# Performance work log

Measured on AMD Instinct MI355X. Metric: run time of the kernel, lower is better.

Reference implementation:

```python
import jax, jax.numpy as jnp
from jax import lax
import numpy as np
import math

ALPHA = 1000.0
BETA = 100.0
K = 24
INIT_DIM = 64
STAGES = 4
NUM_POINTS = 2048
B = 16
EPS = 1e-5


def embedding_spe(x, out_dim):
    # x: [..., in_dim] -> [..., out_dim] sinusoidal embedding
    in_dim = x.shape[-1]
    feat_dim = math.ceil(out_dim / (in_dim * 2))
    dim_embed = jnp.asarray(ALPHA ** (np.arange(feat_dim) / feat_dim), x.dtype)
    feat_num = feat_dim * 2 * in_dim
    out_idx = np.linspace(0, feat_num - 1, out_dim).astype(np.int64)
    div = BETA * x[..., None] / dim_embed            # [..., in_dim, feat_dim]
    pe = jnp.stack([jnp.sin(div), jnp.cos(div)], -1)  # [..., in_dim, feat_dim, 2]
    pe = pe.reshape(x.shape[:-1] + (feat_num,))       # order matches torch cat(flatten(stack))
    return pe[..., out_idx]


def fps_single(xyz, npoint):
    # xyz: [N,3] -> indices [npoint] (deterministic start at index 0)
    n = xyz.shape[0]

    def body(carry, _):
        dist, farthest = carry
        centroid = xyz[farthest]
        d = jnp.sum((xyz - centroid) ** 2, -1)
        dist = jnp.minimum(dist, d)
        nxt = jnp.argmax(dist).astype(jnp.int32)
        return (dist, nxt), farthest

    init = (jnp.full((n,), 1e10, xyz.dtype), jnp.array(0, jnp.int32))
    _, idx = lax.scan(body, init, None, length=npoint)
    return idx


def knn(k, xyz, new_xyz):
    # xyz [B,N,3], new_xyz [B,S,3] -> [B,S,k] indices of k nearest points
    d = (jnp.sum(new_xyz ** 2, -1, keepdims=True)
         + jnp.sum(xyz ** 2, -1)[:, None, :]
         - 2.0 * jnp.einsum('bsc,bnc->bsn', new_xyz, xyz))
    _, idx = lax.top_k(-d, k)
    return idx


def gather(pts, idx):
    # pts [B,N,C], idx [B,...] -> [B,...,C]
    b = pts.shape[0]
    bi = jnp.arange(b).reshape((b,) + (1,) * (idx.ndim - 1))
    return pts[bi, idx]


def stage(xyz, feat, npoint, out_dim, gamma, beta_p):
    fps_idx = jax.vmap(lambda p: fps_single(p, npoint))(lax.stop_gradient(xyz))
    xyz_s = gather(xyz, fps_idx)    # [B,S,3]
    feat_s = gather(feat, fps_idx)  # [B,S,C]
    idx_knn = knn(K, lax.stop_gradient(xyz), lax.stop_gradient(xyz_s))  # [B,S,K]
    xyz_knn = gather(xyz, idx_knn)    # [B,S,K,3]
    feat_knn = gather(feat, idx_knn)  # [B,S,K,C]
    # normalize by global (unbiased) std, like torch.std over whole tensor
    xyz_c = xyz_knn - xyz_s[:, :, None, :]
    xyz_knn = xyz_c / (jnp.std(xyz_c, ddof=1) + 1e-05)
    feat_c = feat_knn - feat_s[:, :, None, :]
    feat_knn = feat_c / (jnp.std(feat_c, ddof=1) + 1e-05)
    bsz, s, k, c = feat_knn.shape
    feat_knn = jnp.concatenate(
        [feat_knn, jnp.broadcast_to(feat_s[:, :, None, :], (bsz, s, k, c))], -1)  # [B,S,K,2C]
    # SPE aggregation
    pe = embedding_spe(xyz_knn, out_dim)
    w = (feat_knn + pe) * pe
    # neighbor pooling: max + mean over K
    agg = jnp.max(w, -2) + jnp.mean(w, -2)  # [B,S,out_dim]
    # BatchNorm1d (training-mode batch stats, biased var) + exact GELU
    mean = jnp.mean(agg, axis=(0, 1))
    var = jnp.var(agg, axis=(0, 1))
    y = gamma * (agg - mean) / jnp.sqrt(var + EPS) + beta_p
    return xyz_s, jax.nn.gelu(y, approximate=False)


def setup_inputs() -> dict:
    key = jax.random.key(0)
    ks = jax.random.split(key, 2)
    inp = {'xyz': jax.random.normal(ks[0], (B, NUM_POINTS, 3), jnp.float32)}
    dim = INIT_DIM
    for i in range(STAGES):
        dim *= 2
        inp[f'gamma{i}'] = jnp.ones((dim,), jnp.float32)
        inp[f'beta{i}'] = jnp.zeros((dim,), jnp.float32)
    return inp


def reference(xyz, gamma0, beta0, gamma1, beta1, gamma2, beta2, gamma3, beta3):
    gammas = [gamma0, gamma1, gamma2, gamma3]
    betas = [beta0, beta1, beta2, beta3]
    feat = embedding_spe(xyz, INIT_DIM)
    npoint, dim = NUM_POINTS, INIT_DIM
    for i in range(STAGES):
        dim *= 2
        npoint //= 2
        xyz, feat = stage(xyz, feat, npoint, dim, gammas[i], betas[i])
    return jnp.max(feat, -2) + jnp.mean(feat, -2)  # [B, 1024]
```

## Files before the change

### kernel.cpp

```cpp
#include <hip/hip_runtime.h>
#include <math.h>

#pragma clang fp contract(off)

static constexpr int BATCH = 16;
static constexpr int NPTS0 = 2048;
static constexpr int KNN = 24;

static constexpr size_t OFF_STATS = 0;
static constexpr size_t OFF_BN    = 256;
static constexpr size_t OFF_DE    = 32768;
static constexpr size_t OFF_MAP   = 36864;
static constexpr size_t OFF_XYZ1  = 49152;
static constexpr size_t OFF_XYZ2  = OFF_XYZ1 + (size_t)16*1024*3*4;
static constexpr size_t OFF_XYZ3  = OFF_XYZ2 + (size_t)16*512*3*4;
static constexpr size_t OFF_XYZ4  = OFF_XYZ3 + (size_t)16*256*3*4;
static constexpr size_t OFF_FPS0  = OFF_XYZ4 + (size_t)16*128*3*4;
static constexpr size_t OFF_FPS1  = OFF_FPS0 + (size_t)16*1024*4;
static constexpr size_t OFF_FPS2  = OFF_FPS1 + (size_t)16*512*4;
static constexpr size_t OFF_FPS3  = OFF_FPS2 + (size_t)16*256*4;
static constexpr size_t OFF_KNN   = OFF_FPS3 + (size_t)16*128*4;
static constexpr size_t OFF_FEATA = OFF_KNN + (size_t)16*1024*24*4;
static constexpr size_t OFF_FEATB = OFF_FEATA + (size_t)16*2048*64*4;
static constexpr size_t OFF_FEATS = OFF_FEATB + (size_t)16*2048*64*4;
static constexpr size_t OFF_AGG   = OFF_FEATS + (size_t)16*1024*64*4;
static constexpr size_t WS_NEED   = OFF_AGG + (size_t)16*1024*128*4;

__device__ inline uint64_t kmax64(uint64_t a, uint64_t b) { return a > b ? a : b; }

template <int CTRL>
__device__ inline uint64_t dpp_shift64(uint64_t k) {
  int hi = (int)(unsigned)(k >> 32), lo = (int)(unsigned)k;
  int oh = __builtin_amdgcn_update_dpp(hi, hi, CTRL, 0xF, 0xF, false);
  int ol = __builtin_amdgcn_update_dpp(lo, lo, CTRL, 0xF, 0xF, false);
  return ((uint64_t)(unsigned)oh << 32) | (unsigned)ol;
}
__device__ inline uint64_t wave_reduce_max64(uint64_t k) {
  k = kmax64(k, dpp_shift64<0x111>(k));
  k = kmax64(k, dpp_shift64<0x112>(k));
  k = kmax64(k, dpp_shift64<0x114>(k));
  k = kmax64(k, dpp_shift64<0x118>(k));
  k = kmax64(k, dpp_shift64<0x142>(k));
  k = kmax64(k, dpp_shift64<0x143>(k));
  return k;
}

__device__ inline unsigned sortable_f32(float f) {
  unsigned b = __float_as_uint(f);
  unsigned m = (unsigned)((int)b >> 31) | 0x80000000u;
  return b ^ m;
}

__device__ inline unsigned med3u(unsigned a, unsigned b, unsigned c) {
  unsigned r;
  asm("v_med3_u32 %0, %1, %2, %3" : "=v"(r) : "v"(a), "v"(b), "v"(c));
  return r;
}

__device__ inline void ins24(unsigned kk[KNN], unsigned v) {
#pragma unroll
  for (int e = KNN - 1; e >= 1; --e) kk[e] = med3u(kk[e - 1], kk[e], v);
  kk[0] = kk[0] < v ? kk[0] : v;
}

__global__ void init_tables(float* __restrict__ de, int* __restrict__ mp) {
  const int outs[5] = {64, 128, 256, 512, 1024};
  const int fds[5]  = {11, 22, 43, 86, 171};
  const int deo[5]  = {0, 11, 33, 76, 162};
  const int mpo[5]  = {0, 64, 192, 448, 960};
  const int tid = threadIdx.x;
  for (int c = 0; c < 5; ++c) {
    const int fd = fds[c], out = outs[c];
    for (int j = tid; j < fd; j += blockDim.x)
      de[deo[c] + j] = (float)pow(1000.0, (double)j / (double)fd);
    const double step = (double)(6 * fd - 1) / (double)(out - 1);
    for (int f = tid; f < out; f += blockDim.x)
      mp[mpo[c] + f] = (int)(step * (double)f);
  }
}

__global__ __launch_bounds__(256) void embed_init(const float* __restrict__ xyz,
                                                  float* __restrict__ feat,
                                                  const float* __restrict__ de,
                                                  const int* __restrict__ mp) {
  int g = blockIdx.x * blockDim.x + threadIdx.x;
  if (g >= BATCH * NPTS0 * 64) return;
  int c = g & 63;
  int bn = g >> 6;
  int m = mp[c];
  int sc = m & 1;
  int a = m >> 1;
  int ci = a / 11;
  int j = a - ci * 11;
  float x = xyz[bn * 3 + ci];
  float ang = (100.0f * x) / de[j];
  feat[g] = sc ? cosf(ang) : sinf(ang);
}

template <int PTS>
__device__ void fps_stage(const float* lds_cur, float* lds_next, int* idx_buf,
                          unsigned* red,
                          int* __restrict__ fps_idx, float* __restrict__ xyz_next) {
  const int S = PTS * 128;
  const int tid = threadIdx.x;
  float px[PTS], py[PTS], pz[PTS], dist[PTS];
#pragma unroll
  for (int p = 0; p < PTS; ++p) {
    int gi = tid + p * 256;
    px[p] = lds_cur[3 * gi];
    py[p] = lds_cur[3 * gi + 1];
    pz[p] = lds_cur[3 * gi + 2];
    dist[p] = 1e10f;
  }
  float cx = lds_cur[0], cy = lds_cur[1], cz = lds_cur[2];
  if (tid == 0) {
    idx_buf[0] = 0;
    lds_next[0] = cx; lds_next[1] = cy; lds_next[2] = cz;
  }
  for (int t = 1; t < S; ++t) {
    float bd = -1.0f;
    int bp = 0;
#pragma unroll
    for (int p = 0; p < PTS; ++p) {
      float dx = px[p] - cx, dy = py[p] - cy, dz = pz[p] - cz;
      float dd = dx * dx + dy * dy;
      dd = dd + dz * dz;
      float nd = fminf(dist[p], dd);
      dist[p] = nd;
      if (nd > bd) { bd = nd; bp = p; }
    }
    unsigned gi = (unsigned)tid + ((unsigned)bp << 8);
    uint64_t key = ((uint64_t)__float_as_uint(bd) << 32) | (~gi);
    key = wave_reduce_max64(key);
    unsigned wlo = (unsigned)__builtin_amdgcn_readlane((int)(unsigned)key, 63);
    unsigned whi = (unsigned)__builtin_amdgcn_readlane((int)(unsigned)(key >> 32), 63);
    unsigned gi_w = ~wlo;
    unsigned pw = gi_w >> 8;
    float wx = px[0], wy = py[0], wz = pz[0];
#pragma unroll
    for (int p = 1; p < PTS; ++p)
      if (pw == (unsigned)p) { wx = px[p]; wy = py[p]; wz = pz[p]; }
    if (tid == (int)(gi_w & 255u)) {
      unsigned* row = red + (t & 1) * 32 + (tid >> 6) * 8;
      row[0] = whi; row[1] = wlo;
      row[2] = __float_as_uint(wx); row[3] = __float_as_uint(wy); row[4] = __float_as_uint(wz);
    }
    __syncthreads();
    const unsigned* rp = red + (t & 1) * 32;
    uint4 q0 = *(const uint4*)(rp + 0);
    uint4 q1 = *(const uint4*)(rp + 8);
    uint4 q2 = *(const uint4*)(rp + 16);
    uint4 q3 = *(const uint4*)(rp + 24);
    unsigned z0 = rp[4], z1 = rp[12], z2 = rp[20], z3 = rp[28];
    uint64_t k0 = ((uint64_t)q0.x << 32) | q0.y;
    uint64_t k1 = ((uint64_t)q1.x << 32) | q1.y;
    uint64_t k2 = ((uint64_t)q2.x << 32) | q2.y;
    uint64_t k3 = ((uint64_t)q3.x << 32) | q3.y;
    bool s01 = k0 >= k1;
    uint64_t ka = s01 ? k0 : k1;
    unsigned xa = s01 ? q0.z : q1.z, ya = s01 ? q0.w : q1.w, za = s01 ? z0 : z1;
    bool s23 = k2 >= k3;
    uint64_t kb = s23 ? k2 : k3;
    unsigned xb = s23 ? q2.z : q3.z, yb = s23 ? q2.w : q3.w, zb = s23 ? z2 : z3;
    bool sab = ka >= kb;
    uint64_t km = sab ? ka : kb;
    cx = __uint_as_float(sab ? xa : xb);
    cy = __uint_as_float(sab ? ya : yb);
    cz = __uint_as_float(sab ? za : zb);
    if (tid == 0) {
      idx_buf[t] = (int)(~(unsigned)km);
      lds_next[3 * t] = cx; lds_next[3 * t + 1] = cy; lds_next[3 * t + 2] = cz;
    }
  }
  __syncthreads();
  for (int u = tid; u < S; u += 256) fps_idx[u] = idx_buf[u];
  for (int u = tid; u < 3 * S; u += 256) xyz_next[u] = lds_next[u];
}

__global__ __launch_bounds__(256) void fps_all(const float* __restrict__ xyz0,
                                               float* __restrict__ xyz1, float* __restrict__ xyz2,
                                               float* __restrict__ xyz3, float* __restrict__ xyz4,
                                               int* __restrict__ i0, int* __restrict__ i1,
                                               int* __restrict__ i2, int* __restrict__ i3) {
  __shared__ float lds[3 * (2048 + 1024 + 512 + 256 + 128)];
  __shared__ int idxb[1024 + 512 + 256 + 128];
  __shared__ __align__(16) unsigned red[2 * 4 * 8];
  const int b = blockIdx.x;
  float* l0 = lds;
  float* l1 = l0 + 3 * 2048;
  float* l2 = l1 + 3 * 1024;
  float* l3 = l2 + 3 * 512;
  float* l4 = l3 + 3 * 256;
  int* ib0 = idxb;
  int* ib1 = ib0 + 1024;
  int* ib2 = ib1 + 512;
  int* ib3 = ib2 + 256;
  for (int t = threadIdx.x; t < 3 * 2048; t += 256) l0[t] = xyz0[(size_t)b * 3 * 2048 + t];
  __syncthreads();
  fps_stage<8>(l0, l1, ib0, red, i0 + b * 1024, xyz1 + (size_t)b * 1024 * 3);
  fps_stage<4>(l1, l2, ib1, red, i1 + b * 512, xyz2 + (size_t)b * 512 * 3);
  fps_stage<2>(l2, l3, ib2, red, i2 + b * 256, xyz3 + (size_t)b * 256 * 3);
  fps_stage<1>(l3, l4, ib3, red, i3 + b * 128, xyz4 + (size_t)b * 128 * 3);
}

static constexpr int MGS = 29;
__global__ __launch_bounds__(256) void knn_tau(const float* __restrict__ db_xyz,
                                               const float* __restrict__ q_xyz,
                                               unsigned* __restrict__ tau,
                                               int Np, int S) {
  extern __shared__ float smem[];
  float4* db = (float4*)smem;
  unsigned* mg = (unsigned*)(db + Np);
  const int tid = threadIdx.x, lane = tid & 63, wv = tid >> 6;
  const int bpb = S >> 6;
  const int b = blockIdx.x / bpb;
  const int qbase = (blockIdx.x % bpb) * 64;
  for (int j = tid; j < Np; j += 256) {
    float x = db_xyz[((size_t)b * Np + j) * 3 + 0];
    float y = db_xyz[((size_t)b * Np + j) * 3 + 1];
    float z = db_xyz[((size_t)b * Np + j) * 3 + 2];
    float pn = x * x + y * y;
    pn = pn + z * z;
    db[j] = make_float4(x, y, z, pn);
  }
  __syncthreads();
  const int s = qbase + lane;
  float qx = q_xyz[((size_t)b * S + s) * 3 + 0];
  float qy = q_xyz[((size_t)b * S + s) * 3 + 1];
  float qz = q_xyz[((size_t)b * S + s) * 3 + 2];
  float qn = qx * qx + qy * qy;
  qn = qn + qz * qz;
  unsigned kk[KNN];
#pragma unroll
  for (int e = 0; e < KNN; ++e) kk[e] = 0xFFFFFFFFu;
  const int cpw = Np >> 2;
  const int beg = wv * cpw, end = beg + cpw;
  for (int j0 = beg; j0 < end; j0 += 8) {
    float4 p[8];
#pragma unroll
    for (int u = 0; u < 8; ++u) p[u] = db[j0 + u];
#pragma unroll
    for (int u = 0; u < 8; ++u) {
      float dot = fmaf(qz, p[u].z, fmaf(qy, p[u].y, qx * p[u].x));
      float d = (qn + p[u].w) - 2.0f * dot;
      unsigned su = sortable_f32(d);
      if (__any(su < kk[KNN - 1])) ins24(kk, su);
    }
  }
  unsigned* myrow = mg + (wv * 64 + lane) * MGS;
#pragma unroll
  for (int e = 0; e < KNN; ++e) myrow[e] = kk[e];
  __syncthreads();
  if (wv == 0) {
    for (int w = 1; w < 4; ++w) {
      const unsigned* orow = mg + (w * 64 + lane) * MGS;
#pragma unroll
      for (int e = 0; e < KNN; ++e) {
        unsigned v = orow[e];
        if (__any(v < kk[KNN - 1])) ins24(kk, v);
      }
    }
    tau[(size_t)b * S + s] = kk[KNN - 1];
  }
}

__global__ __launch_bounds__(256) void knn_collect(const float* __restrict__ db_xyz,
                                                   const float* __restrict__ q_xyz,
                                                   const unsigned* __restrict__ tau,
                                                   int* __restrict__ out_idx,
                                                   int Np, int S) {
  __shared__ uint64_t bufA[4][24];
  __shared__ uint64_t bufB[4][24];
  const int lane = threadIdx.x & 63, wv = threadIdx.x >> 6;
  const int qi = blockIdx.x * 4 + wv;
  const int b = qi / S, s = qi % S;
  float qx = q_xyz[((size_t)b * S + s) * 3 + 0];
  float qy = q_xyz[((size_t)b * S + s) * 3 + 1];
  float qz = q_xyz[((size_t)b * S + s) * 3 + 2];
  float qn = qx * qx + qy * qy;
  qn = qn + qz * qz;
  const unsigned tt = tau[qi];
  int cntA = 0, cntB = 0;
  const unsigned long long lmlt = (1ull << lane) - 1;
  const int iters = Np >> 6;
  for (int it = 0; it < iters; ++it) {
    int j = it * 64 + lane;
    float x = db_xyz[((size_t)b * Np + j) * 3 + 0];
    float y = db_xyz[((size_t)b * Np + j) * 3 + 1];
    float z = db_xyz[((size_t)b * Np + j) * 3 + 2];
    float pn = x * x + y * y;
    pn = pn + z * z;
    float dot = fmaf(qz, z, fmaf(qy, y, qx * x));
    float d = (qn + pn) - 2.0f * dot;
    unsigned su = sortable_f32(d);
    unsigned long long mlt = __ballot(su < tt);
    unsigned long long meq = __ballot(su == tt);
    if (mlt) {
      int pos = cntA + __popcll(mlt & lmlt);
      if (su < tt && pos < 24) bufA[wv][pos] = ((uint64_t)su << 32) | (unsigned)j;
      cntA += __popcll(mlt);
    }
    if (meq) {
      int pos = cntB + __popcll(meq & lmlt);
      if (su == tt && pos < 24) bufB[wv][pos] = ((uint64_t)su << 32) | (unsigned)j;
      cntB += __popcll(meq);
    }
  }
  uint64_t v = (lane < cntA) ? bufA[wv][lane] : ~0ull;
#pragma unroll
  for (int k = 2; k <= 64; k <<= 1) {
#pragma unroll
    for (int m = k >> 1; m > 0; m >>= 1) {
      uint64_t o = __shfl_xor(v, m);
      bool takemin = (((lane & k) == 0) == ((lane & m) == 0));
      uint64_t mn = v < o ? v : o;
      uint64_t mx = v < o ? o : v;
      v = takemin ? mn : mx;
    }
  }
  if (lane < KNN) {
    uint64_t key = (lane < cntA) ? v : bufB[wv][lane - cntA];
    out_idx[(size_t)qi * KNN + lane] = (int)(unsigned)key;
  }
}

__global__ __launch_bounds__(256) void gather_feat_s(const float* __restrict__ feat,
                                                     const int* __restrict__ fidx,
                                                     float* __restrict__ out, int Np, int S, int C) {
  int g = blockIdx.x * blockDim.x + threadIdx.x;
  if (g >= BATCH * S * C) return;
  int c = g % C;
  int bs = g / C;
  int s = bs % S;
  int b = bs / S;
  int src = fidx[b * S + s];
  out[g] = feat[((size_t)b * Np + src) * C + c];
}

__global__ __launch_bounds__(256) void center_reduce(const float* __restrict__ xyz,
                                                     const float* __restrict__ xyz_s,
                                                     const float* __restrict__ feat,
                                                     const float* __restrict__ feat_s,
                                                     const int* __restrict__ kidx,
                                                     double* __restrict__ sums,
                                                     int Np, int S, int C) {
  int g = blockIdx.x * blockDim.x + threadIdx.x;
  int total = BATCH * S * KNN;
  double sx = 0, sxx = 0, sf = 0, sff = 0;
  if (g < total) {
    int bs = g / KNN;
    int s = bs % S;
    int b = bs / S;
    int j = kidx[g];
    const float* pc = xyz + ((size_t)b * Np + j) * 3;
    const float* qc = xyz_s + ((size_t)b * S + s) * 3;
    for (int c = 0; c < 3; ++c) {
      float v = pc[c] - qc[c];
      sx += (double)v;
      sxx += (double)v * (double)v;
    }
    const float4* fr = (const float4*)(feat + ((size_t)b * Np + j) * C);
    const float4* fs = (const float4*)(feat_s + ((size_t)b * S + s) * C);
    for (int c = 0; c < C / 4; ++c) {
      float4 a = fr[c], bq = fs[c];
      float v0 = a.x - bq.x, v1 = a.y - bq.y, v2 = a.z - bq.z, v3 = a.w - bq.w;
      sf += (double)v0 + (double)v1 + (double)v2 + (double)v3;
      sff += (double)v0 * v0 + (double)v1 * v1 + (double)v2 * v2 + (double)v3 * v3;
    }
  }
#pragma unroll
  for (int m = 1; m < 64; m <<= 1) {
    sx += __shfl_xor(sx, m);
    sxx += __shfl_xor(sxx, m);
    sf += __shfl_xor(sf, m);
    sff += __shfl_xor(sff, m);
  }
  __shared__ double part[4][4];
  int wv = threadIdx.x >> 6;
  if ((threadIdx.x & 63) == 0) { part[wv][0] = sx; part[wv][1] = sxx; part[wv][2] = sf; part[wv][3] = sff; }
  __syncthreads();
  if (threadIdx.x == 0) {
    double a = 0, b2 = 0, c2 = 0, d2 = 0;
    for (int w = 0; w < 4; ++w) { a += part[w][0]; b2 += part[w][1]; c2 += part[w][2]; d2 += part[w][3]; }
    atomicAdd(&sums[0], a);
    atomicAdd(&sums[1], b2);
    atomicAdd(&sums[2], c2);
    atomicAdd(&sums[3], d2);
  }
}

template <int CH>
__global__ __launch_bounds__(256) void agg_kernel(const float* __restrict__ xyz,
                                                  const float* __restrict__ xyz_s,
                                                  const float* __restrict__ feat,
                                                  const float* __restrict__ feat_s,
                                                  const int* __restrict__ kidx,
                                                  const double* __restrict__ csums,
                                                  const float* __restrict__ de,
                                                  const int* __restrict__ mp,
                                                  float* __restrict__ agg,
                                                  int Np, int S, int C, int fd,
                                                  double nx_d, double nf_d) {
  const int lane = threadIdx.x & 63;
  const int wv = threadIdx.x >> 6;
  const int q = blockIdx.x * 4 + wv;
  const int s = q % S;
  const int b = q / S;
  double sxd = csums[0], sxxd = csums[1], sfd = csums[2], sffd = csums[3];
  float stdx = sqrtf((float)((sxxd - sxd * sxd / nx_d) / (nx_d - 1.0)));
  float stdf = sqrtf((float)((sffd - sfd * sfd / nf_d) / (nf_d - 1.0)));
  float invx = 1.0f / (stdx + 1e-5f);
  float invf = 1.0f / (stdf + 1e-5f);
  float cx = xyz_s[((size_t)b * S + s) * 3 + 0];
  float cy = xyz_s[((size_t)b * S + s) * 3 + 1];
  float cz = xyz_s[((size_t)b * S + s) * 3 + 2];
  const float* fsrow = feat_s + ((size_t)b * S + s) * C;
  int ci[CH];
  float dev[CH], fsv[CH];
  bool issin[CH], fh[CH];
#pragma unroll
  for (int ch = 0; ch < CH; ++ch) {
    int f = ch * 64 + lane;
    int m = mp[f];
    issin[ch] = (m & 1) == 0;
    int a = m >> 1;
    int cc = a / fd;
    ci[ch] = cc;
    dev[ch] = de[a - cc * fd];
    fh[ch] = f < C;
    fsv[ch] = fh[ch] ? fsrow[f] : fsrow[f - C];
  }
  float wmax[CH], wsum[CH];
#pragma unroll
  for (int ch = 0; ch < CH; ++ch) { wmax[ch] = -3.4e38f; wsum[ch] = 0.f; }
  const int* krow = kidx + ((size_t)b * S + s) * KNN;
  for (int k = 0; k < KNN; ++k) {
    int j = krow[k];
    const float* pr = xyz + ((size_t)b * Np + j) * 3;
    float n0 = (pr[0] - cx) * invx;
    float n1 = (pr[1] - cy) * invx;
    float n2 = (pr[2] - cz) * invx;
    const float* fr = feat + ((size_t)b * Np + j) * C;
#pragma unroll
    for (int ch = 0; ch < CH; ++ch) {
      float xv = (ci[ch] == 0) ? n0 : ((ci[ch] == 1) ? n1 : n2);
      float ang = (100.0f * xv) / dev[ch];
      float sv, cv;
      sincosf(ang, &sv, &cv);
      float pef = issin[ch] ? sv : cv;
      int f = ch * 64 + lane;
      float val = fh[ch] ? (fr[f] - fsv[ch]) * invf : fsv[ch];
      float w = (val + pef) * pef;
      wmax[ch] = fmaxf(wmax[ch], w);
      wsum[ch] += w;
    }
  }
  float* arow = agg + (size_t)q * (CH * 64);
#pragma unroll
  for (int ch = 0; ch < CH; ++ch) {
    int f = ch * 64 + lane;
    arow[f] = wmax[ch] + wsum[ch] / (float)KNN;
  }
}

__global__ __launch_bounds__(256) void bn_reduce(const float* __restrict__ agg,
                                                 double* __restrict__ bns,
                                                 int R, int D) {
  int r0 = blockIdx.x * 64;
  for (int c = threadIdx.x; c < D; c += 256) {
    double s = 0, ss = 0;
    for (int r = 0; r < 64; ++r) {
      float v = agg[(size_t)(r0 + r) * D + c];
      s += (double)v;
      ss += (double)v * (double)v;
    }
    atomicAdd(&bns[c], s);
    atomicAdd(&bns[D + c], ss);
  }
}

__global__ __launch_bounds__(256) void bn_apply(const float* __restrict__ agg,
                                                const double* __restrict__ bns,
                                                const float* __restrict__ gamma,
                                                const float* __restrict__ beta,
                                                float* __restrict__ outf, int R, int D) {
  int g = blockIdx.x * blockDim.x + threadIdx.x;
  if (g >= R * D) return;
  int c = g % D;
  double n = (double)R;
  double mu = bns[c] / n;
  double var = bns[D + c] / n - mu * mu;
  float mean = (float)mu;
  float rstd = 1.0f / sqrtf((float)var + 1e-5f);
  float x = (agg[g] - mean) * rstd;
  float y = gamma[c] * x + beta[c];
  float e = erff(y * 0.70710678118654752440f);
  outf[g] = 0.5f * y * (1.0f + e);
}

__global__ __launch_bounds__(256) void final_kernel(const float* __restrict__ feat,
                                                    float* __restrict__ out) {
  int g = blockIdx.x * blockDim.x + threadIdx.x;
  if (g >= BATCH * 1024) return;
  int f = g % 1024;
  int b = g / 1024;
  const float* base = feat + (size_t)b * 128 * 1024 + f;
  float mx = -3.4e38f;
  float sm = 0.f;
  for (int s = 0; s < 128; ++s) {
    float v = base[(size_t)s * 1024];
    mx = fmaxf(mx, v);
    sm += v;
  }
  out[g] = mx + sm / 128.0f;
}

extern "C" void kernel_launch(void* const* d_in, const int* in_sizes, int n_in,
                              void* d_out, int out_size, void* d_ws, size_t ws_size,
                              hipStream_t stream) {
  (void)in_sizes; (void)n_in; (void)out_size;
  if (ws_size < WS_NEED) return;
  const float* xyz = (const float*)d_in[0];
  const float* gam[4] = {(const float*)d_in[1], (const float*)d_in[3], (const float*)d_in[5], (const float*)d_in[7]};
  const float* bet[4] = {(const float*)d_in[2], (const float*)d_in[4], (const float*)d_in[6], (const float*)d_in[8]};
  char* ws = (char*)d_ws;
  double* stats = (double*)(ws + OFF_STATS);
  double* bns = (double*)(ws + OFF_BN);
  float* de = (float*)(ws + OFF_DE);
  int* mp = (int*)(ws + OFF_MAP);
  float* xyz1 = (float*)(ws + OFF_XYZ1);
  float* xyz2 = (float*)(ws + OFF_XYZ2);
  float* xyz3 = (float*)(ws + OFF_XYZ3);
  float* xyz4 = (float*)(ws + OFF_XYZ4);
  int* fpsI[4] = {(int*)(ws + OFF_FPS0), (int*)(ws + OFF_FPS1), (int*)(ws + OFF_FPS2), (int*)(ws + OFF_FPS3)};
  int* kidx = (int*)(ws + OFF_KNN);
  float* feata = (float*)(ws + OFF_FEATA);
  float* featb = (float*)(ws + OFF_FEATB);
  float* feats = (float*)(ws + OFF_FEATS);
  unsigned* tau = (unsigned*)(ws + OFF_FEATS);
  float* agg = (float*)(ws + OFF_AGG);

  hipMemsetAsync(ws, 0, 32768, stream);
  init_tables<<<1, 256, 0, stream>>>(de, mp);
  fps_all<<<16, 256, 0, stream>>>(xyz, xyz1, xyz2, xyz3, xyz4, fpsI[0], fpsI[1], fpsI[2], fpsI[3]);
  embed_init<<<(BATCH * NPTS0 * 64) / 256, 256, 0, stream>>>(xyz, feata, de, mp);

  const int Ns[4] = {2048, 1024, 512, 256};
  const int Cs[4] = {64, 128, 256, 512};
  const int fdv[4] = {22, 43, 86, 171};
  const int deo[4] = {11, 33, 76, 162};
  const int mpo[4] = {64, 192, 448, 960};
  const float* xin[5] = {xyz, xyz1, xyz2, xyz3, xyz4};
  float* fcur = feata;
  float* fnext = featb;
  int bnoff = 0;
  for (int i = 0; i < 4; ++i) {
    const int Np = Ns[i], S = Np / 2, C = Cs[i], D = 2 * C;
    size_t tau_lds = (size_t)Np * 16 + (size_t)4 * 64 * MGS * 4;
    knn_tau<<<16 * (S / 64), 256, tau_lds, stream>>>(xin[i], xin[i + 1], tau, Np, S);
    knn_collect<<<(BATCH * S) / 4, 256, 0, stream>>>(xin[i], xin[i + 1], tau, kidx, Np, S);
    gather_feat_s<<<(BATCH * S * C) / 256, 256, 0, stream>>>(fcur, fpsI[i], feats, Np, S, C);
    const int tuples = BATCH * S * KNN;
    center_reduce<<<(tuples + 255) / 256, 256, 0, stream>>>(xin[i], xin[i + 1], fcur, feats, kidx,
                                                            stats + 4 * i, Np, S, C);
    double nx = (double)tuples * 3.0;
    double nf = (double)tuples * (double)C;
    dim3 ag((BATCH * S) / 4);
    switch (D / 64) {
      case 2:
        agg_kernel<2><<<ag, 256, 0, stream>>>(xin[i], xin[i + 1], fcur, feats, kidx, stats + 4 * i,
                                              de + deo[i], mp + mpo[i], agg, Np, S, C, fdv[i], nx, nf);
        break;
      case 4:
        agg_kernel<4><<<ag, 256, 0, stream>>>(xin[i], xin[i + 1], fcur, feats, kidx, stats + 4 * i,
                                              de + deo[i], mp + mpo[i], agg, Np, S, C, fdv[i], nx, nf);
        break;
      case 8:
        agg_kernel<8><<<ag, 256, 0, stream>>>(xin[i], xin[i + 1], fcur, feats, kidx, stats + 4 * i,
                                              de + deo[i], mp + mpo[i], agg, Np, S, C, fdv[i], nx, nf);
        break;
      default:
        agg_kernel<16><<<ag, 256, 0, stream>>>(xin[i], xin[i + 1], fcur, feats, kidx, stats + 4 * i,
                                               de + deo[i], mp + mpo[i], agg, Np, S, C, fdv[i], nx, nf);
        break;
    }
    const int R = BATCH * S;
    bn_reduce<<<R / 64, 256, 0, stream>>>(agg, bns + bnoff, R, D);
    bn_apply<<<(R * D) / 256, 256, 0, stream>>>(agg, bns + bnoff, gam[i], bet[i], fnext, R, D);
    bnoff += 2 * D;
    float* t = fcur; fcur = fnext; fnext = t;
  }
  final_kernel<<<(BATCH * 1024) / 256, 256, 0, stream>>>(fcur, (float*)d_out);
}
```

Measured before the change: 2.155 ms.

## Replace FPS block barrier with LDS flag spin-sync and pack two batches per block

The farthest-point-sampling kernel now carries the winner's coordinates through the DPP wave reduction instead of broadcasting the winning lane and selecting them afterwards. The per-iteration __syncthreads is replaced by per-wave LDS flags that each wave spins on. Two batches now share one 512-thread block, each half synchronising independently, so the two halves no longer wait on each other's barrier. The aim is to cut barrier latency on the serial FPS chain. The trade-off is that spin-waiting on volatile LDS flags costs issue slots and relies on memory-ordering assumptions. Also, running 8 blocks instead of 16 means fewer CUs are used.

```diff
diff --git a/kernel.cpp b/kernel.cpp
--- a/kernel.cpp
+++ b/kernel.cpp
@@ -26,25 +26,6 @@
 static constexpr size_t OFF_AGG   = OFF_FEATS + (size_t)16*1024*64*4;
 static constexpr size_t WS_NEED   = OFF_AGG + (size_t)16*1024*128*4;
 
-__device__ inline uint64_t kmax64(uint64_t a, uint64_t b) { return a > b ? a : b; }
-
-template <int CTRL>
-__device__ inline uint64_t dpp_shift64(uint64_t k) {
-  int hi = (int)(unsigned)(k >> 32), lo = (int)(unsigned)k;
-  int oh = __builtin_amdgcn_update_dpp(hi, hi, CTRL, 0xF, 0xF, false);
-  int ol = __builtin_amdgcn_update_dpp(lo, lo, CTRL, 0xF, 0xF, false);
-  return ((uint64_t)(unsigned)oh << 32) | (unsigned)ol;
-}
-__device__ inline uint64_t wave_reduce_max64(uint64_t k) {
-  k = kmax64(k, dpp_shift64<0x111>(k));
-  k = kmax64(k, dpp_shift64<0x112>(k));
-  k = kmax64(k, dpp_shift64<0x114>(k));
-  k = kmax64(k, dpp_shift64<0x118>(k));
-  k = kmax64(k, dpp_shift64<0x142>(k));
-  k = kmax64(k, dpp_shift64<0x143>(k));
-  return k;
-}
-
 __device__ inline unsigned sortable_f32(float f) {
   unsigned b = __float_as_uint(f);
   unsigned m = (unsigned)((int)b >> 31) | 0x80000000u;
@@ -61,6 +42,26 @@
 #pragma unroll
   for (int e = KNN - 1; e >= 1; --e) kk[e] = med3u(kk[e - 1], kk[e], v);
   kk[0] = kk[0] < v ? kk[0] : v;
+}
+
+template <int CTRL>
+__device__ inline unsigned dpp1(unsigned v) {
+  return (unsigned)__builtin_amdgcn_update_dpp((int)v, (int)v, CTRL, 0xF, 0xF, false);
+}
+
+struct R5 { uint64_t k; unsigned x, y, z; };
+
+template <int CTRL>
+__device__ inline void red5_step(R5& r) {
+  unsigned khi = (unsigned)(r.k >> 32), klo = (unsigned)r.k;
+  unsigned shi = dpp1<CTRL>(khi), slo = dpp1<CTRL>(klo);
+  unsigned sx = dpp1<CTRL>(r.x), sy = dpp1<CTRL>(r.y), sz = dpp1<CTRL>(r.z);
+  uint64_t sk = ((uint64_t)shi << 32) | slo;
+  if (sk > r.k) { r.k = sk; r.x = sx; r.y = sy; r.z = sz; }
+}
+__device__ inline void red5_wave(R5& r) {
+  red5_step<0x111>(r); red5_step<0x112>(r); red5_step<0x114>(r);
+  red5_step<0x118>(r); red5_step<0x142>(r); red5_step<0x143>(r);
 }
 
 __global__ void init_tables(float* __restrict__ de, int* __restrict__ mp) {
@@ -99,25 +100,25 @@
 
 template <int PTS>
 __device__ void fps_stage(const float* lds_cur, float* lds_next, int* idx_buf,
-                          unsigned* red,
-                          int* __restrict__ fps_idx, float* __restrict__ xyz_next) {
+                          unsigned* rows, volatile unsigned* flags, unsigned& gt,
+                          int htid, int* __restrict__ fps_idx, float* __restrict__ xyz_next) {
   const int S = PTS * 128;
-  const int tid = threadIdx.x;
+  const int lane = htid & 63, wv = htid >> 6;
   float px[PTS], py[PTS], pz[PTS], dist[PTS];
 #pragma unroll
   for (int p = 0; p < PTS; ++p) {
-    int gi = tid + p * 256;
+    int gi = htid + p * 256;
     px[p] = lds_cur[3 * gi];
     py[p] = lds_cur[3 * gi + 1];
     pz[p] = lds_cur[3 * gi + 2];
     dist[p] = 1e10f;
   }
   float cx = lds_cur[0], cy = lds_cur[1], cz = lds_cur[2];
-  if (tid == 0) {
+  if (htid == 0) {
     idx_buf[0] = 0;
     lds_next[0] = cx; lds_next[1] = cy; lds_next[2] = cz;
   }
-  for (int t = 1; t < S; ++t) {
+  for (int t = 1; t < S; ++t, ++gt) {
     float bd = -1.0f;
     int bp = 0;
 #pragma unroll
@@ -129,24 +130,29 @@
       dist[p] = nd;
       if (nd > bd) { bd = nd; bp = p; }
     }
-    unsigned gi = (unsigned)tid + ((unsigned)bp << 8);
-    uint64_t key = ((uint64_t)__float_as_uint(bd) << 32) | (~gi);
-    key = wave_reduce_max64(key);
-    unsigned wlo = (unsigned)__builtin_amdgcn_readlane((int)(unsigned)key, 63);
-    unsigned whi = (unsigned)__builtin_amdgcn_readlane((int)(unsigned)(key >> 32), 63);
-    unsigned gi_w = ~wlo;
-    unsigned pw = gi_w >> 8;
+    unsigned gi = (unsigned)htid + ((unsigned)bp << 8);
+    R5 r;
+    r.k = ((uint64_t)__float_as_uint(bd) << 32) | (~gi);
     float wx = px[0], wy = py[0], wz = pz[0];
 #pragma unroll
     for (int p = 1; p < PTS; ++p)
-      if (pw == (unsigned)p) { wx = px[p]; wy = py[p]; wz = pz[p]; }
-    if (tid == (int)(gi_w & 255u)) {
-      unsigned* row = red + (t & 1) * 32 + (tid >> 6) * 8;
-      row[0] = whi; row[1] = wlo;
-      row[2] = __float_as_uint(wx); row[3] = __float_as_uint(wy); row[4] = __float_as_uint(wz);
-    }
-    __syncthreads();
-    const unsigned* rp = red + (t & 1) * 32;
+      if (bp == p) { wx = px[p]; wy = py[p]; wz = pz[p]; }
+    r.x = __float_as_uint(wx); r.y = __float_as_uint(wy); r.z = __float_as_uint(wz);
+    red5_wave(r);
+    const unsigned par = gt & 1u;
+    unsigned* row = rows + (par * 4 + (unsigned)wv) * 8;
+    if (lane == 63) {
+      *(uint4*)row = make_uint4((unsigned)(r.k >> 32), (unsigned)r.k, r.x, r.y);
+      row[4] = r.z;
+    }
+    asm volatile("s_waitcnt lgkmcnt(0)" ::: "memory");
+    if (lane == 63) flags[wv] = gt;
+    for (;;) {
+      unsigned f0 = flags[0], f1 = flags[1], f2 = flags[2], f3 = flags[3];
+      if (f0 >= gt && f1 >= gt && f2 >= gt && f3 >= gt) break;
+    }
+    asm volatile("" ::: "memory");
+    const unsigned* rp = rows + par * 32;
     uint4 q0 = *(const uint4*)(rp + 0);
     uint4 q1 = *(const uint4*)(rp + 8);
     uint4 q2 = *(const uint4*)(rp + 16);
@@ -167,40 +173,54 @@
     cx = __uint_as_float(sab ? xa : xb);
     cy = __uint_as_float(sab ? ya : yb);
     cz = __uint_as_float(sab ? za : zb);
-    if (tid == 0) {
+    if (htid == 0) {
       idx_buf[t] = (int)(~(unsigned)km);
       lds_next[3 * t] = cx; lds_next[3 * t + 1] = cy; lds_next[3 * t + 2] = cz;
     }
   }
-  __syncthreads();
-  for (int u = tid; u < S; u += 256) fps_idx[u] = idx_buf[u];
-  for (int u = tid; u < 3 * S; u += 256) xyz_next[u] = lds_next[u];
-}
-
-__global__ __launch_bounds__(256) void fps_all(const float* __restrict__ xyz0,
+  asm volatile("s_waitcnt lgkmcnt(0)" ::: "memory");
+  if (lane == 63) flags[wv] = gt;
+  for (;;) {
+    unsigned f0 = flags[0], f1 = flags[1], f2 = flags[2], f3 = flags[3];
+    if (f0 >= gt && f1 >= gt && f2 >= gt && f3 >= gt) break;
+  }
+  asm volatile("" ::: "memory");
+  ++gt;
+  for (int u = htid; u < S; u += 256) fps_idx[u] = idx_buf[u];
+  for (int u = htid; u < 3 * S; u += 256) xyz_next[u] = lds_next[u];
+}
+
+__global__ __launch_bounds__(512) void fps_all(const float* __restrict__ xyz0,
                                                float* __restrict__ xyz1, float* __restrict__ xyz2,
                                                float* __restrict__ xyz3, float* __restrict__ xyz4,
                                                int* __restrict__ i0, int* __restrict__ i1,
                                                int* __restrict__ i2, int* __restrict__ i3) {
-  __shared__ float lds[3 * (2048 + 1024 + 512 + 256 + 128)];
-  __shared__ int idxb[1024 + 512 + 256 + 128];
-  __shared__ __align__(16) unsigned red[2 * 4 * 8];
-  const int b = blockIdx.x;
-  float* l0 = lds;
+  __shared__ float lds[2][3 * (2048 + 1024 + 512 + 256 + 128)];
+  __shared__ int idxb[2][1024 + 512 + 256 + 128];
+  __shared__ __align__(16) unsigned rows[2][2 * 4 * 8];
+  __shared__ unsigned flagsArr[2][8];
+  const int half = threadIdx.x >> 8;
+  const int htid = threadIdx.x & 255;
+  const int b = blockIdx.x * 2 + half;
+  float* l0 = lds[half];
   float* l1 = l0 + 3 * 2048;
   float* l2 = l1 + 3 * 1024;
   float* l3 = l2 + 3 * 512;
   float* l4 = l3 + 3 * 256;
-  int* ib0 = idxb;
+  int* ib0 = idxb[half];
   int* ib1 = ib0 + 1024;
   int* ib2 = ib1 + 512;
   int* ib3 = ib2 + 256;
-  for (int t = threadIdx.x; t < 3 * 2048; t += 256) l0[t] = xyz0[(size_t)b * 3 * 2048 + t];
+  volatile unsigned* flags = flagsArr[half];
+  if (htid < 4) flags[htid] = 0u;
+  for (int t = htid; t < 3 * 2048; t += 256) l0[t] = xyz0[(size_t)b * 3 * 2048 + t];
   __syncthreads();
-  fps_stage<8>(l0, l1, ib0, red, i0 + b * 1024, xyz1 + (size_t)b * 1024 * 3);
-  fps_stage<4>(l1, l2, ib1, red, i1 + b * 512, xyz2 + (size_t)b * 512 * 3);
-  fps_stage<2>(l2, l3, ib2, red, i2 + b * 256, xyz3 + (size_t)b * 256 * 3);
-  fps_stage<1>(l3, l4, ib3, red, i3 + b * 128, xyz4 + (size_t)b * 128 * 3);
+  if (half == 1) __builtin_amdgcn_s_sleep(8);
+  unsigned gt = 1;
+  fps_stage<8>(l0, l1, ib0, rows[half], flags, gt, htid, i0 + b * 1024, xyz1 + (size_t)b * 1024 * 3);
+  fps_stage<4>(l1, l2, ib1, rows[half], flags, gt, htid, i1 + b * 512, xyz2 + (size_t)b * 512 * 3);
+  fps_stage<2>(l2, l3, ib2, rows[half], flags, gt, htid, i2 + b * 256, xyz3 + (size_t)b * 256 * 3);
+  fps_stage<1>(l3, l4, ib3, rows[half], flags, gt, htid, i3 + b * 128, xyz4 + (size_t)b * 128 * 3);
 }
 
 static constexpr int MGS = 29;
@@ -542,7 +562,7 @@
 
   hipMemsetAsync(ws, 0, 32768, stream);
   init_tables<<<1, 256, 0, stream>>>(de, mp);
-  fps_all<<<16, 256, 0, stream>>>(xyz, xyz1, xyz2, xyz3, xyz4, fpsI[0], fpsI[1], fpsI[2], fpsI[3]);
+  fps_all<<<8, 512, 0, stream>>>(xyz, xyz1, xyz2, xyz3, xyz4, fpsI[0], fpsI[1], fpsI[2], fpsI[3]);
   embed_init<<<(BATCH * NPTS0 * 64) / 256, 256, 0, stream>>>(xyz, feata, de, mp);
 
   const int Ns[4] = {2048, 1024, 512, 256};
```

Result: slower. 2.683 ms (+24.5%).
